# Optimization experiments

Hardware: AMD Instinct MI355X
Metric: run time of the kernel (lower is better)

The kernel has to match this reference:

```python
import jax, jax.numpy as jnp
import numpy as np

N, E, D_IN, HEADS, C = 100000, 1600000, 128, 4, 32  # C = out_channels per head


def setup_inputs() -> dict:
    key = jax.random.key(0)
    ks = jax.random.split(key, 10)
    s = 1.0 / np.sqrt(D_IN)
    return {
        "x": jax.random.normal(ks[0], (N, D_IN), jnp.float32),
        "edge_index": jax.random.randint(ks[1], (2, E), 0, N, jnp.int64),
        "Wq": jax.random.normal(ks[2], (D_IN, HEADS * C), jnp.float32) * s,
        "bq": jnp.zeros((HEADS * C,), jnp.float32),
        "Wk": jax.random.normal(ks[3], (D_IN, HEADS * C), jnp.float32) * s,
        "bk": jnp.zeros((HEADS * C,), jnp.float32),
        "Wv": jax.random.normal(ks[4], (D_IN, HEADS * C), jnp.float32) * s,
        "bv": jnp.zeros((HEADS * C,), jnp.float32),
        "Wskip": jax.random.normal(ks[5], (D_IN, HEADS * C), jnp.float32) * s,
        "bskip": jnp.zeros((HEADS * C,), jnp.float32),
    }


def reference(x, edge_index, Wq, bq, Wk, bk, Wv, bv, Wskip, bskip):
    n = x.shape[0]
    src, dst = edge_index[0], edge_index[1]  # message flows src (j) -> dst (i)
    q = (x @ Wq + bq).reshape(n, HEADS, C)
    k = (x @ Wk + bk).reshape(n, HEADS, C)
    v = (x @ Wv + bv).reshape(n, HEADS, C)

    # per-edge attention logits [E, H]
    alpha = jnp.einsum('ehc,ehc->eh', q[dst], k[src]) / jnp.sqrt(jnp.float32(C))

    # segment softmax over incoming edges of each target node
    m = jax.ops.segment_max(alpha, dst, num_segments=n)          # [N, H]
    p = jnp.exp(alpha - m[dst])                                   # [E, H]
    z = jax.ops.segment_sum(p, dst, num_segments=n)               # [N, H]
    w = p / (z[dst] + 1e-16)                                      # [E, H]

    # softmax-weighted scatter aggregation of values
    out = jax.ops.segment_sum(v[src] * w[:, :, None], dst, num_segments=n)
    out = out.reshape(n, HEADS * C)

    # root/skip connection (beta=False default: plain add)
    out = out + x @ Wskip + bskip
    return out
```

## Files before the change

### kernel.cpp

```cpp
#include <hip/hip_runtime.h>

#define DIN 128
#define NHEADS 4
#define CH 32
#define MT 128
#define CHUNK 4096
#define NPB 256
#define EPB_IT 25

#define ST_H 136

typedef _Float16 h8 __attribute__((ext_vector_type(8)));
typedef _Float16 h2 __attribute__((ext_vector_type(2)));
typedef float f4 __attribute__((ext_vector_type(4)));

__global__ __launch_bounds__(256) void prep_w(
    const float* __restrict__ Wq, const float* __restrict__ Wk,
    const float* __restrict__ Wv, const float* __restrict__ Wsk,
    _Float16* __restrict__ wt)
{
    int i = blockIdx.x * 256 + threadIdx.x;
    if (i >= 4 * 16384) return;
    int mat = i >> 14;
    int rem = i & 16383;
    int n  = rem >> 7;
    int kk = rem & 127;
    const float* W = (mat == 0) ? Wq : (mat == 1) ? Wk : (mat == 2) ? Wv : Wsk;
    wt[i] = (_Float16)W[kk * 128 + n];
}

__global__ __launch_bounds__(256) void qkvs_mat(
    const float* __restrict__ x, const _Float16* __restrict__ wt,
    const float* __restrict__ bq, const float* __restrict__ bk,
    const float* __restrict__ bv, const float* __restrict__ bsk,
    _Float16* __restrict__ qh, _Float16* __restrict__ kvh,
    _Float16* __restrict__ skiph, int N)
{
    __shared__ _Float16 Sbuf[17408];
    const int t = threadIdx.x;
    const int mat = blockIdx.x;
    const int rowBase = blockIdx.y * MT;

    for (int i = t; i < MT * 16; i += 256) {
        int r  = i >> 4;
        int c8 = i & 15;
        int gr = rowBase + r;
        _Float16 h[8];
        if (gr < N) {
            float4 f0 = reinterpret_cast<const float4*>(x)[(size_t)gr * 32 + c8 * 2];
            float4 f1 = reinterpret_cast<const float4*>(x)[(size_t)gr * 32 + c8 * 2 + 1];
            h[0] = (_Float16)f0.x; h[1] = (_Float16)f0.y;
            h[2] = (_Float16)f0.z; h[3] = (_Float16)f0.w;
            h[4] = (_Float16)f1.x; h[5] = (_Float16)f1.y;
            h[6] = (_Float16)f1.z; h[7] = (_Float16)f1.w;
        } else {
            #pragma unroll
            for (int j = 0; j < 8; ++j) h[j] = (_Float16)0.f;
        }
        *reinterpret_cast<uint4*>(&Sbuf[r * 128 + ((c8 ^ (r & 7)) << 3)]) =
            *reinterpret_cast<uint4*>(h);
    }
    __syncthreads();

    const int wid  = t >> 6;
    const int l    = t & 63;
    const int lm   = l & 15;
    const int quad = l >> 4;

    const _Float16* __restrict__ Bsrc = wt + (size_t)mat * 16384;

    f4 acc[2][8];
    #pragma unroll
    for (int ms = 0; ms < 2; ++ms)
        #pragma unroll
        for (int nt = 0; nt < 8; ++nt)
            acc[ms][nt] = (f4){0.f, 0.f, 0.f, 0.f};

    #pragma unroll
    for (int kq = 0; kq < 4; ++kq) {
        const int c8 = kq * 4 + quad;
        const int k0 = c8 << 3;
        h8 a0 = *reinterpret_cast<const h8*>(
            &Sbuf[(wid * 32 + lm) * 128 + ((c8 ^ (lm & 7)) << 3)]);
        h8 a1 = *reinterpret_cast<const h8*>(
            &Sbuf[(wid * 32 + 16 + lm) * 128 + ((c8 ^ (lm & 7)) << 3)]);
        #pragma unroll
        for (int nt = 0; nt < 8; ++nt) {
            h8 b = *reinterpret_cast<const h8*>(
                &Bsrc[(size_t)(nt * 16 + lm) * 128 + k0]);
            acc[0][nt] = __builtin_amdgcn_mfma_f32_16x16x32_f16(a0, b, acc[0][nt], 0, 0, 0);
            acc[1][nt] = __builtin_amdgcn_mfma_f32_16x16x32_f16(a1, b, acc[1][nt], 0, 0, 0);
        }
    }
    __syncthreads();

    const float* bias = (mat == 0) ? bq : (mat == 1) ? bk : (mat == 2) ? bv : bsk;

    #pragma unroll
    for (int ms = 0; ms < 2; ++ms) {
        #pragma unroll
        for (int nt = 0; nt < 8; ++nt) {
            int col = nt * 16 + lm;
            float bsv = bias[col];
            int row = wid * 32 + ms * 16 + quad * 4;
            #pragma unroll
            for (int i2 = 0; i2 < 4; ++i2)
                Sbuf[(row + i2) * ST_H + col] = (_Float16)(acc[ms][nt][i2] + bsv);
        }
    }
    __syncthreads();

    if (mat == 0 || mat == 3) {
        _Float16* __restrict__ dst = (mat == 0) ? qh : skiph;
        for (int j = t; j < 2048; j += 256) {
            int r  = j >> 4;
            int c0 = (j & 15) << 3;
            int gr = rowBase + r;
            if (gr < N)
                *reinterpret_cast<uint4*>(&dst[(size_t)gr * 128 + c0]) =
                    *reinterpret_cast<const uint4*>(&Sbuf[r * ST_H + c0]);
        }
    } else {
        const int koff = (mat == 2) ? 4 : 0;
        for (int j = t; j < 4096; j += 256) {
            int r = j >> 5;
            int g = j & 31;
            int gr = rowBase + r;
            if (gr < N)
                *reinterpret_cast<uint2*>(&kvh[(size_t)gr * 256 + g * 8 + koff]) =
                    *reinterpret_cast<const uint2*>(&Sbuf[r * ST_H + g * 4]);
        }
    }
}

__global__ __launch_bounds__(256) void bucket_hist(
    const int* __restrict__ ei, int* __restrict__ bcnt, int E, int nb)
{
    __shared__ int lds[512];
    for (int b = threadIdx.x; b < nb; b += 256) lds[b] = 0;
    __syncthreads();
    for (long long i = (long long)blockIdx.x * 256 + threadIdx.x; i < E;
         i += (long long)gridDim.x * 256)
        atomicAdd(&lds[ei[(size_t)E + i] >> 8], 1);
    __syncthreads();
    for (int b = threadIdx.x; b < nb; b += 256)
        if (lds[b]) atomicAdd(&bcnt[b], lds[b]);
}

__global__ __launch_bounds__(512) void scan_buckets(
    const int* __restrict__ bcnt, int* __restrict__ boff,
    int* __restrict__ bcur, int nb)
{
    __shared__ int ws[8];
    int t = threadIdx.x, lane = t & 63, wid = t >> 6;
    int v = (t < nb) ? bcnt[t] : 0;
    int s = v;
    #pragma unroll
    for (int off = 1; off < 64; off <<= 1) {
        int n = __shfl_up(s, off);
        if (lane >= off) s += n;
    }
    if (lane == 63) ws[wid] = s;
    __syncthreads();
    int add = 0;
    for (int w = 0; w < wid; ++w) add += ws[w];
    int excl = s - v + add;
    if (t < nb) { boff[t] = excl; bcur[t] = excl; }
    if (t == nb - 1) boff[nb] = excl + v;
}

__global__ __launch_bounds__(256) void bucket_scatter(
    const int* __restrict__ ei, int* __restrict__ bcur,
    uint2* __restrict__ pairs, int E, int nb)
{
    __shared__ int cnt[512];
    int t = threadIdx.x;
    for (int b = t; b < nb; b += 256) cnt[b] = 0;
    __syncthreads();

    long long e0 = (long long)blockIdx.x * (256 * EPB_IT);
    int ps[EPB_IT], pd[EPB_IT];
    #pragma unroll
    for (int j = 0; j < EPB_IT; ++j) {
        long long e = e0 + j * 256 + t;
        if (e < E) {
            ps[j] = ei[e];
            pd[j] = ei[(size_t)E + e];
            atomicAdd(&cnt[pd[j] >> 8], 1);
        } else pd[j] = -1;
    }
    __syncthreads();
    for (int b = t; b < nb; b += 256) {
        int c = cnt[b];
        if (c) cnt[b] = atomicAdd(&bcur[b], c);
    }
    __syncthreads();
    #pragma unroll
    for (int j = 0; j < EPB_IT; ++j) {
        if (pd[j] >= 0) {
            int pos = atomicAdd(&cnt[pd[j] >> 8], 1);
            pairs[pos] = make_uint2((unsigned)ps[j], (unsigned)pd[j]);
        }
    }
}

__global__ __launch_bounds__(256) void bucket_counts(
    const uint2* __restrict__ pairs, const int* __restrict__ boff,
    int* __restrict__ counts, int N)
{
    __shared__ int cnt[NPB];
    int b = blockIdx.x, t = threadIdx.x;
    cnt[t] = 0;
    __syncthreads();
    int s = boff[b], e = boff[b + 1];
    for (int i = s + t; i < e; i += 256)
        atomicAdd(&cnt[pairs[i].y & (NPB - 1)], 1);
    __syncthreads();
    int node = b * NPB + t;
    if (node < N) counts[node] = cnt[t];
}

__global__ __launch_bounds__(256) void chunk_sums(
    const int* __restrict__ counts, int* __restrict__ partials, int N)
{
    int b = blockIdx.x, t = threadIdx.x;
    int base = b * CHUNK + t * 16;
    int s = 0;
    #pragma unroll
    for (int j = 0; j < 16; ++j) {
        int i = base + j;
        if (i < N) s += counts[i];
    }
    #pragma unroll
    for (int off = 1; off < 64; off <<= 1) s += __shfl_xor(s, off);
    __shared__ int ws[4];
    int lane = t & 63, wid = t >> 6;
    if (lane == 0) ws[wid] = s;
    __syncthreads();
    if (t == 0) partials[b] = ws[0] + ws[1] + ws[2] + ws[3];
}

__global__ __launch_bounds__(256) void scan_chunks(
    const int* __restrict__ partials, int* __restrict__ chunkoff, int nch)
{
    __shared__ int ws[4];
    int t = threadIdx.x, lane = t & 63, wid = t >> 6;
    int v = (t < nch) ? partials[t] : 0;
    int s = v;
    #pragma unroll
    for (int off = 1; off < 64; off <<= 1) {
        int n = __shfl_up(s, off);
        if (lane >= off) s += n;
    }
    if (lane == 63) ws[wid] = s;
    __syncthreads();
    int add = 0;
    for (int w = 0; w < wid; ++w) add += ws[w];
    if (t < nch) chunkoff[t] = s - v + add;
}

__global__ __launch_bounds__(256) void scan_write(
    const int* __restrict__ counts, const int* __restrict__ chunkoff,
    int* __restrict__ rowptr, int N)
{
    int b = blockIdx.x, t = threadIdx.x;
    int base = b * CHUNK + t * 16;
    int vals[16];
    int s = 0;
    #pragma unroll
    for (int j = 0; j < 16; ++j) {
        int i = base + j;
        vals[j] = (i < N) ? counts[i] : 0;
        s += vals[j];
    }
    int lane = t & 63, wid = t >> 6;
    int incl = s;
    #pragma unroll
    for (int off = 1; off < 64; off <<= 1) {
        int n = __shfl_up(incl, off);
        if (lane >= off) incl += n;
    }
    __shared__ int ws[4];
    if (lane == 63) ws[wid] = incl;
    __syncthreads();
    int add = chunkoff[b];
    for (int w = 0; w < wid; ++w) add += ws[w];
    int run = incl - s + add;
    #pragma unroll
    for (int j = 0; j < 16; ++j) {
        int i = base + j;
        if (i < N) rowptr[i + 1] = run + vals[j];
        run += vals[j];
    }
    if (b == 0 && t == 0) rowptr[0] = 0;
}

__global__ __launch_bounds__(256) void bucket_place(
    const uint2* __restrict__ pairs, const int* __restrict__ boff,
    const int* __restrict__ rowptr, int* __restrict__ sorted, int N)
{
    __shared__ int cur[NPB];
    int b = blockIdx.x, t = threadIdx.x;
    int node = b * NPB + t;
    cur[t] = (node < N) ? rowptr[node] : 0;
    __syncthreads();
    int s = boff[b], e = boff[b + 1];
    for (int i = s + t; i < e; i += 256) {
        uint2 pr = pairs[i];
        int pos = atomicAdd(&cur[pr.y & (NPB - 1)], 1);
        sorted[pos] = (int)pr.x;
    }
}

__device__ inline float4 cvt4(unsigned lo, unsigned hi) {
    union { unsigned u[2]; _Float16 h[4]; } c;
    c.u[0] = lo; c.u[1] = hi;
    return make_float4((float)c.h[0], (float)c.h[1], (float)c.h[2], (float)c.h[3]);
}

__device__ inline h2 as_h2(unsigned u) {
    union { unsigned u; h2 h; } c;
    c.u = u;
    return c.h;
}

__global__ __launch_bounds__(256) void node_aggregate(
    const _Float16* __restrict__ q, const _Float16* __restrict__ kv,
    const _Float16* __restrict__ skiph,
    const int* __restrict__ rowptr, const int* __restrict__ srcs,
    float* __restrict__ out, int N)
{
    int gid  = blockIdx.x * 256 + threadIdx.x;
    int node = gid >> 5;
    if (node >= N) return;
    int l = gid & 31;

    uint2 qu = reinterpret_cast<const uint2*>(q + (size_t)node * 128)[l];
    h2 qa = as_h2(qu.x), qb = as_h2(qu.y);

    float4 acc = make_float4(0.f, 0.f, 0.f, 0.f);
    float z = 0.f;

    const uint4* kv4 = reinterpret_cast<const uint4*>(kv);
    const float SC = 0.17677669529663687f;
    int e0 = rowptr[node], e1 = rowptr[node + 1];
    int e = e0;

    for (; e + 8 <= e1; e += 8) {
        int s[8];
        #pragma unroll
        for (int j = 0; j < 8; ++j) s[j] = srcs[e + j];
        uint4 r[8];
        #pragma unroll
        for (int j = 0; j < 8; ++j) r[j] = kv4[(size_t)s[j] * 32 + l];

        float sv[8];
        #pragma unroll
        for (int j = 0; j < 8; ++j) {
            sv[j] = __builtin_amdgcn_fdot2(qa, as_h2(r[j].x),
                    __builtin_amdgcn_fdot2(qb, as_h2(r[j].y), 0.f, false), false);
        }
        #pragma unroll
        for (int j = 0; j < 8; ++j) sv[j] += __shfl_xor(sv[j], 1);
        #pragma unroll
        for (int j = 0; j < 8; ++j) sv[j] += __shfl_xor(sv[j], 2);
        #pragma unroll
        for (int j = 0; j < 8; ++j) sv[j] += __shfl_xor(sv[j], 4);

        #pragma unroll
        for (int j = 0; j < 8; ++j) {
            float p = __expf(sv[j] * SC);
            float4 v = cvt4(r[j].z, r[j].w);
            z += p;
            acc.x += p * v.x; acc.y += p * v.y;
            acc.z += p * v.z; acc.w += p * v.w;
        }
    }
    for (; e + 4 <= e1; e += 4) {
        int s0 = srcs[e], s1 = srcs[e + 1], s2 = srcs[e + 2], s3 = srcs[e + 3];
        uint4 r0 = kv4[(size_t)s0 * 32 + l];
        uint4 r1 = kv4[(size_t)s1 * 32 + l];
        uint4 r2 = kv4[(size_t)s2 * 32 + l];
        uint4 r3 = kv4[(size_t)s3 * 32 + l];
        float sa = __builtin_amdgcn_fdot2(qa, as_h2(r0.x),
                   __builtin_amdgcn_fdot2(qb, as_h2(r0.y), 0.f, false), false);
        float sb = __builtin_amdgcn_fdot2(qa, as_h2(r1.x),
                   __builtin_amdgcn_fdot2(qb, as_h2(r1.y), 0.f, false), false);
        float sc = __builtin_amdgcn_fdot2(qa, as_h2(r2.x),
                   __builtin_amdgcn_fdot2(qb, as_h2(r2.y), 0.f, false), false);
        float sd = __builtin_amdgcn_fdot2(qa, as_h2(r3.x),
                   __builtin_amdgcn_fdot2(qb, as_h2(r3.y), 0.f, false), false);
        sa += __shfl_xor(sa, 1); sb += __shfl_xor(sb, 1);
        sc += __shfl_xor(sc, 1); sd += __shfl_xor(sd, 1);
        sa += __shfl_xor(sa, 2); sb += __shfl_xor(sb, 2);
        sc += __shfl_xor(sc, 2); sd += __shfl_xor(sd, 2);
        sa += __shfl_xor(sa, 4); sb += __shfl_xor(sb, 4);
        sc += __shfl_xor(sc, 4); sd += __shfl_xor(sd, 4);
        float pa = __expf(sa * SC), pb = __expf(sb * SC);
        float pc = __expf(sc * SC), pdd = __expf(sd * SC);
        float4 v0 = cvt4(r0.z, r0.w);
        float4 v1 = cvt4(r1.z, r1.w);
        float4 v2 = cvt4(r2.z, r2.w);
        float4 v3 = cvt4(r3.z, r3.w);
        z += (pa + pb) + (pc + pdd);
        acc.x += pa * v0.x + pb * v1.x + pc * v2.x + pdd * v3.x;
        acc.y += pa * v0.y + pb * v1.y + pc * v2.y + pdd * v3.y;
        acc.z += pa * v0.z + pb * v1.z + pc * v2.z + pdd * v3.z;
        acc.w += pa * v0.w + pb * v1.w + pc * v2.w + pdd * v3.w;
    }
    for (; e < e1; ++e) {
        int s0 = srcs[e];
        uint4 r0 = kv4[(size_t)s0 * 32 + l];
        float sa = __builtin_amdgcn_fdot2(qa, as_h2(r0.x),
                   __builtin_amdgcn_fdot2(qb, as_h2(r0.y), 0.f, false), false);
        sa += __shfl_xor(sa, 1);
        sa += __shfl_xor(sa, 2);
        sa += __shfl_xor(sa, 4);
        float pa = __expf(sa * SC);
        float4 v0 = cvt4(r0.z, r0.w);
        z += pa;
        acc.x += pa * v0.x; acc.y += pa * v0.y;
        acc.z += pa * v0.z; acc.w += pa * v0.w;
    }

    uint2 su = reinterpret_cast<const uint2*>(skiph + (size_t)node * 128)[l];
    float4 sk = cvt4(su.x, su.y);
    float inv = 1.f / (z + 1e-16f);
    float4 o;
    o.x = sk.x + acc.x * inv; o.y = sk.y + acc.y * inv;
    o.z = sk.z + acc.z * inv; o.w = sk.w + acc.w * inv;
    reinterpret_cast<float4*>(out)[(size_t)node * 32 + l] = o;
}

extern "C" void kernel_launch(void* const* d_in, const int* in_sizes, int n_in,
                              void* d_out, int out_size, void* d_ws, size_t ws_size,
                              hipStream_t stream)
{
    const float* x   = (const float*)d_in[0];
    const int*   ei  = (const int*)d_in[1];
    const float* Wq  = (const float*)d_in[2];
    const float* bq  = (const float*)d_in[3];
    const float* Wk  = (const float*)d_in[4];
    const float* bk  = (const float*)d_in[5];
    const float* Wv  = (const float*)d_in[6];
    const float* bv  = (const float*)d_in[7];
    const float* Wsk = (const float*)d_in[8];
    const float* bsk = (const float*)d_in[9];
    float* out = (float*)d_out;

    const int N = in_sizes[0] / DIN;
    const int E = in_sizes[1] / 2;
    const int nb = (N + NPB - 1) / NPB;

    _Float16* qh    = (_Float16*)d_ws;
    _Float16* kvh   = qh + (size_t)N * DIN;
    _Float16* skiph = kvh + (size_t)N * 256;
    _Float16* wt    = skiph + (size_t)N * DIN;
    uint2* pairs  = (uint2*)(wt + 4 * 16384);
    int* sorted   = (int*)(pairs + (size_t)E);
    int* counts   = sorted + E;
    int* rowptr   = counts + N;
    int* bcnt     = rowptr + (N + 1);
    int* boff     = bcnt + 512;
    int* bcur     = boff + 513;
    int* partials = bcur + 512;
    int* chunkoff = partials + 256;

    hipMemsetAsync(bcnt, 0, 512 * sizeof(int), stream);

    prep_w<<<(4 * 16384 + 255) / 256, 256, 0, stream>>>(Wq, Wk, Wv, Wsk, wt);

    dim3 ggrid(4, (N + MT - 1) / MT);
    qkvs_mat<<<ggrid, 256, 0, stream>>>(x, wt, bq, bk, bv, bsk,
                                        qh, kvh, skiph, N);

    bucket_hist<<<256, 256, 0, stream>>>(ei, bcnt, E, nb);
    scan_buckets<<<1, 512, 0, stream>>>(bcnt, boff, bcur, nb);
    int sb = (E + 256 * EPB_IT - 1) / (256 * EPB_IT);
    bucket_scatter<<<sb, 256, 0, stream>>>(ei, bcur, pairs, E, nb);
    bucket_counts<<<nb, 256, 0, stream>>>(pairs, boff, counts, N);

    int nch = (N + CHUNK - 1) / CHUNK;
    chunk_sums<<<nch, 256, 0, stream>>>(counts, partials, N);
    scan_chunks<<<1, 256, 0, stream>>>(partials, chunkoff, nch);
    scan_write<<<nch, 256, 0, stream>>>(counts, chunkoff, rowptr, N);

    bucket_place<<<nb, 256, 0, stream>>>(pairs, boff, rowptr, sorted, N);

    int ab = (N * 32 + 255) / 256;
    node_aggregate<<<ab, 256, 0, stream>>>(qh, kvh, skiph, rowptr, sorted, out, N);
}
```

Measured before the change: 413.2 us.

## Fuse bucket count, scan and placement into one kernel; split K/V buffers

Replaces the five-kernel CSR build (bucket_counts, chunk_sums, scan_chunks, scan_write, bucket_place) with a single bucket_finalize kernel. Each bucket computes its per-node counts, scans them locally and places edges, using the bucket's global offset as the base. Edge pairs are packed into one 32-bit word (src<<8 | dst low byte), which halves scatter and read traffic but assumes src fits in 24 bits. It also splits the interleaved K/V layout into separate K and V arrays, so each edge now needs two 8-byte gathers instead of one 16-byte gather, and it drops the 4-wide tail loop in aggregation.

```diff
diff --git a/kernel.cpp b/kernel.cpp
--- a/kernel.cpp
+++ b/kernel.cpp
@@ -4,7 +4,6 @@
 #define NHEADS 4
 #define CH 32
 #define MT 128
-#define CHUNK 4096
 #define NPB 256
 #define EPB_IT 25
 
@@ -33,8 +32,8 @@
     const float* __restrict__ x, const _Float16* __restrict__ wt,
     const float* __restrict__ bq, const float* __restrict__ bk,
     const float* __restrict__ bv, const float* __restrict__ bsk,
-    _Float16* __restrict__ qh, _Float16* __restrict__ kvh,
-    _Float16* __restrict__ skiph, int N)
+    _Float16* __restrict__ qh, _Float16* __restrict__ kh,
+    _Float16* __restrict__ vh, _Float16* __restrict__ skiph, int N)
 {
     __shared__ _Float16 Sbuf[17408];
     const int t = threadIdx.x;
@@ -110,26 +109,15 @@
     }
     __syncthreads();
 
-    if (mat == 0 || mat == 3) {
-        _Float16* __restrict__ dst = (mat == 0) ? qh : skiph;
-        for (int j = t; j < 2048; j += 256) {
-            int r  = j >> 4;
-            int c0 = (j & 15) << 3;
-            int gr = rowBase + r;
-            if (gr < N)
-                *reinterpret_cast<uint4*>(&dst[(size_t)gr * 128 + c0]) =
-                    *reinterpret_cast<const uint4*>(&Sbuf[r * ST_H + c0]);
-        }
-    } else {
-        const int koff = (mat == 2) ? 4 : 0;
-        for (int j = t; j < 4096; j += 256) {
-            int r = j >> 5;
-            int g = j & 31;
-            int gr = rowBase + r;
-            if (gr < N)
-                *reinterpret_cast<uint2*>(&kvh[(size_t)gr * 256 + g * 8 + koff]) =
-                    *reinterpret_cast<const uint2*>(&Sbuf[r * ST_H + g * 4]);
-        }
+    _Float16* __restrict__ dst = (mat == 0) ? qh : (mat == 1) ? kh
+                               : (mat == 2) ? vh : skiph;
+    for (int j = t; j < 2048; j += 256) {
+        int r  = j >> 4;
+        int c0 = (j & 15) << 3;
+        int gr = rowBase + r;
+        if (gr < N)
+            *reinterpret_cast<uint4*>(&dst[(size_t)gr * 128 + c0]) =
+                *reinterpret_cast<const uint4*>(&Sbuf[r * ST_H + c0]);
     }
 }
 
@@ -171,7 +159,7 @@
 
 __global__ __launch_bounds__(256) void bucket_scatter(
     const int* __restrict__ ei, int* __restrict__ bcur,
-    uint2* __restrict__ pairs, int E, int nb)
+    unsigned* __restrict__ pairs, int E, int nb)
 {
     __shared__ int cnt[512];
     int t = threadIdx.x;
@@ -199,116 +187,50 @@
     for (int j = 0; j < EPB_IT; ++j) {
         if (pd[j] >= 0) {
             int pos = atomicAdd(&cnt[pd[j] >> 8], 1);
-            pairs[pos] = make_uint2((unsigned)ps[j], (unsigned)pd[j]);
-        }
-    }
-}
-
-__global__ __launch_bounds__(256) void bucket_counts(
-    const uint2* __restrict__ pairs, const int* __restrict__ boff,
-    int* __restrict__ counts, int N)
+            pairs[pos] = ((unsigned)ps[j] << 8) | ((unsigned)pd[j] & 255u);
+        }
+    }
+}
+
+__global__ __launch_bounds__(256) void bucket_finalize(
+    const unsigned* __restrict__ pairs, const int* __restrict__ boff,
+    int* __restrict__ rowptr, int* __restrict__ sorted, int N, int nb)
 {
     __shared__ int cnt[NPB];
+    __shared__ int cur[NPB];
+    __shared__ int ws[4];
     int b = blockIdx.x, t = threadIdx.x;
     cnt[t] = 0;
     __syncthreads();
-    int s = boff[b], e = boff[b + 1];
-    for (int i = s + t; i < e; i += 256)
-        atomicAdd(&cnt[pairs[i].y & (NPB - 1)], 1);
-    __syncthreads();
-    int node = b * NPB + t;
-    if (node < N) counts[node] = cnt[t];
-}
-
-__global__ __launch_bounds__(256) void chunk_sums(
-    const int* __restrict__ counts, int* __restrict__ partials, int N)
-{
-    int b = blockIdx.x, t = threadIdx.x;
-    int base = b * CHUNK + t * 16;
-    int s = 0;
-    #pragma unroll
-    for (int j = 0; j < 16; ++j) {
-        int i = base + j;
-        if (i < N) s += counts[i];
-    }
-    #pragma unroll
-    for (int off = 1; off < 64; off <<= 1) s += __shfl_xor(s, off);
-    __shared__ int ws[4];
+    int s0 = boff[b], e0 = boff[b + 1];
+    for (int i = s0 + t; i < e0; i += 256)
+        atomicAdd(&cnt[pairs[i] & (NPB - 1)], 1);
+    __syncthreads();
+
+    int v = cnt[t];
     int lane = t & 63, wid = t >> 6;
-    if (lane == 0) ws[wid] = s;
-    __syncthreads();
-    if (t == 0) partials[b] = ws[0] + ws[1] + ws[2] + ws[3];
-}
-
-__global__ __launch_bounds__(256) void scan_chunks(
-    const int* __restrict__ partials, int* __restrict__ chunkoff, int nch)
-{
-    __shared__ int ws[4];
-    int t = threadIdx.x, lane = t & 63, wid = t >> 6;
-    int v = (t < nch) ? partials[t] : 0;
-    int s = v;
-    #pragma unroll
-    for (int off = 1; off < 64; off <<= 1) {
-        int n = __shfl_up(s, off);
-        if (lane >= off) s += n;
-    }
-    if (lane == 63) ws[wid] = s;
-    __syncthreads();
-    int add = 0;
-    for (int w = 0; w < wid; ++w) add += ws[w];
-    if (t < nch) chunkoff[t] = s - v + add;
-}
-
-__global__ __launch_bounds__(256) void scan_write(
-    const int* __restrict__ counts, const int* __restrict__ chunkoff,
-    int* __restrict__ rowptr, int N)
-{
-    int b = blockIdx.x, t = threadIdx.x;
-    int base = b * CHUNK + t * 16;
-    int vals[16];
-    int s = 0;
-    #pragma unroll
-    for (int j = 0; j < 16; ++j) {
-        int i = base + j;
-        vals[j] = (i < N) ? counts[i] : 0;
-        s += vals[j];
-    }
-    int lane = t & 63, wid = t >> 6;
-    int incl = s;
+    int incl = v;
     #pragma unroll
     for (int off = 1; off < 64; off <<= 1) {
         int n = __shfl_up(incl, off);
         if (lane >= off) incl += n;
     }
-    __shared__ int ws[4];
     if (lane == 63) ws[wid] = incl;
     __syncthreads();
-    int add = chunkoff[b];
+    int add = 0;
     for (int w = 0; w < wid; ++w) add += ws[w];
-    int run = incl - s + add;
-    #pragma unroll
-    for (int j = 0; j < 16; ++j) {
-        int i = base + j;
-        if (i < N) rowptr[i + 1] = run + vals[j];
-        run += vals[j];
-    }
-    if (b == 0 && t == 0) rowptr[0] = 0;
-}
-
-__global__ __launch_bounds__(256) void bucket_place(
-    const uint2* __restrict__ pairs, const int* __restrict__ boff,
-    const int* __restrict__ rowptr, int* __restrict__ sorted, int N)
-{
-    __shared__ int cur[NPB];
-    int b = blockIdx.x, t = threadIdx.x;
+    int base = s0 + (incl - v) + add;
+
     int node = b * NPB + t;
-    cur[t] = (node < N) ? rowptr[node] : 0;
-    __syncthreads();
-    int s = boff[b], e = boff[b + 1];
-    for (int i = s + t; i < e; i += 256) {
-        uint2 pr = pairs[i];
-        int pos = atomicAdd(&cur[pr.y & (NPB - 1)], 1);
-        sorted[pos] = (int)pr.x;
+    if (node < N) rowptr[node] = base;
+    if (b == nb - 1 && t == 0) rowptr[N] = boff[nb];
+    cur[t] = base;
+    __syncthreads();
+
+    for (int i = s0 + t; i < e0; i += 256) {
+        unsigned pr = pairs[i];
+        int pos = atomicAdd(&cur[pr & (NPB - 1)], 1);
+        sorted[pos] = (int)(pr >> 8);
     }
 }
 
@@ -325,8 +247,8 @@
 }
 
 __global__ __launch_bounds__(256) void node_aggregate(
-    const _Float16* __restrict__ q, const _Float16* __restrict__ kv,
-    const _Float16* __restrict__ skiph,
+    const _Float16* __restrict__ q, const _Float16* __restrict__ kh,
+    const _Float16* __restrict__ vh, const _Float16* __restrict__ skiph,
     const int* __restrict__ rowptr, const int* __restrict__ srcs,
     float* __restrict__ out, int N)
 {
@@ -341,7 +263,8 @@
     float4 acc = make_float4(0.f, 0.f, 0.f, 0.f);
     float z = 0.f;
 
-    const uint4* kv4 = reinterpret_cast<const uint4*>(kv);
+    const uint2* k2 = reinterpret_cast<const uint2*>(kh);
+    const uint2* v2 = reinterpret_cast<const uint2*>(vh);
     const float SC = 0.17677669529663687f;
     int e0 = rowptr[node], e1 = rowptr[node + 1];
     int e = e0;
@@ -350,15 +273,17 @@
         int s[8];
         #pragma unroll
         for (int j = 0; j < 8; ++j) s[j] = srcs[e + j];
-        uint4 r[8];
-        #pragma unroll
-        for (int j = 0; j < 8; ++j) r[j] = kv4[(size_t)s[j] * 32 + l];
+        uint2 kr[8], vr[8];
+        #pragma unroll
+        for (int j = 0; j < 8; ++j) kr[j] = k2[(size_t)s[j] * 32 + l];
+        #pragma unroll
+        for (int j = 0; j < 8; ++j) vr[j] = v2[(size_t)s[j] * 32 + l];
 
         float sv[8];
         #pragma unroll
         for (int j = 0; j < 8; ++j) {
-            sv[j] = __builtin_amdgcn_fdot2(qa, as_h2(r[j].x),
-                    __builtin_amdgcn_fdot2(qb, as_h2(r[j].y), 0.f, false), false);
+            sv[j] = __builtin_amdgcn_fdot2(qa, as_h2(kr[j].x),
+                    __builtin_amdgcn_fdot2(qb, as_h2(kr[j].y), 0.f, false), false);
         }
         #pragma unroll
         for (int j = 0; j < 8; ++j) sv[j] += __shfl_xor(sv[j], 1);
@@ -370,54 +295,23 @@
         #pragma unroll
         for (int j = 0; j < 8; ++j) {
             float p = __expf(sv[j] * SC);
-            float4 v = cvt4(r[j].z, r[j].w);
+            float4 v = cvt4(vr[j].x, vr[j].y);
             z += p;
             acc.x += p * v.x; acc.y += p * v.y;
             acc.z += p * v.z; acc.w += p * v.w;
         }
     }
-    for (; e + 4 <= e1; e += 4) {
-        int s0 = srcs[e], s1 = srcs[e + 1], s2 = srcs[e + 2], s3 = srcs[e + 3];
-        uint4 r0 = kv4[(size_t)s0 * 32 + l];
-        uint4 r1 = kv4[(size_t)s1 * 32 + l];
-        uint4 r2 = kv4[(size_t)s2 * 32 + l];
-        uint4 r3 = kv4[(size_t)s3 * 32 + l];
-        float sa = __builtin_amdgcn_fdot2(qa, as_h2(r0.x),
-                   __builtin_amdgcn_fdot2(qb, as_h2(r0.y), 0.f, false), false);
-        float sb = __builtin_amdgcn_fdot2(qa, as_h2(r1.x),
-                   __builtin_amdgcn_fdot2(qb, as_h2(r1.y), 0.f, false), false);
-        float sc = __builtin_amdgcn_fdot2(qa, as_h2(r2.x),
-                   __builtin_amdgcn_fdot2(qb, as_h2(r2.y), 0.f, false), false);
-        float sd = __builtin_amdgcn_fdot2(qa, as_h2(r3.x),
-                   __builtin_amdgcn_fdot2(qb, as_h2(r3.y), 0.f, false), false);
-        sa += __shfl_xor(sa, 1); sb += __shfl_xor(sb, 1);
-        sc += __shfl_xor(sc, 1); sd += __shfl_xor(sd, 1);
-        sa += __shfl_xor(sa, 2); sb += __shfl_xor(sb, 2);
-        sc += __shfl_xor(sc, 2); sd += __shfl_xor(sd, 2);
-        sa += __shfl_xor(sa, 4); sb += __shfl_xor(sb, 4);
-        sc += __shfl_xor(sc, 4); sd += __shfl_xor(sd, 4);
-        float pa = __expf(sa * SC), pb = __expf(sb * SC);
-        float pc = __expf(sc * SC), pdd = __expf(sd * SC);
-        float4 v0 = cvt4(r0.z, r0.w);
-        float4 v1 = cvt4(r1.z, r1.w);
-        float4 v2 = cvt4(r2.z, r2.w);
-        float4 v3 = cvt4(r3.z, r3.w);
-        z += (pa + pb) + (pc + pdd);
-        acc.x += pa * v0.x + pb * v1.x + pc * v2.x + pdd * v3.x;
-        acc.y += pa * v0.y + pb * v1.y + pc * v2.y + pdd * v3.y;
-        acc.z += pa * v0.z + pb * v1.z + pc * v2.z + pdd * v3.z;
-        acc.w += pa * v0.w + pb * v1.w + pc * v2.w + pdd * v3.w;
-    }
     for (; e < e1; ++e) {
         int s0 = srcs[e];
-        uint4 r0 = kv4[(size_t)s0 * 32 + l];
-        float sa = __builtin_amdgcn_fdot2(qa, as_h2(r0.x),
-                   __builtin_amdgcn_fdot2(qb, as_h2(r0.y), 0.f, false), false);
+        uint2 kr = k2[(size_t)s0 * 32 + l];
+        uint2 vr = v2[(size_t)s0 * 32 + l];
+        float sa = __builtin_amdgcn_fdot2(qa, as_h2(kr.x),
+                   __builtin_amdgcn_fdot2(qb, as_h2(kr.y), 0.f, false), false);
         sa += __shfl_xor(sa, 1);
         sa += __shfl_xor(sa, 2);
         sa += __shfl_xor(sa, 4);
         float pa = __expf(sa * SC);
-        float4 v0 = cvt4(r0.z, r0.w);
+        float4 v0 = cvt4(vr.x, vr.y);
         z += pa;
         acc.x += pa * v0.x; acc.y += pa * v0.y;
         acc.z += pa * v0.z; acc.w += pa * v0.w;
@@ -453,18 +347,16 @@
     const int nb = (N + NPB - 1) / NPB;
 
     _Float16* qh    = (_Float16*)d_ws;
-    _Float16* kvh   = qh + (size_t)N * DIN;
-    _Float16* skiph = kvh + (size_t)N * 256;
+    _Float16* kh    = qh + (size_t)N * DIN;
+    _Float16* vh    = kh + (size_t)N * DIN;
+    _Float16* skiph = vh + (size_t)N * DIN;
     _Float16* wt    = skiph + (size_t)N * DIN;
-    uint2* pairs  = (uint2*)(wt + 4 * 16384);
+    unsigned* pairs = (unsigned*)(wt + 4 * 16384);
     int* sorted   = (int*)(pairs + (size_t)E);
-    int* counts   = sorted + E;
-    int* rowptr   = counts + N;
+    int* rowptr   = sorted + E;
     int* bcnt     = rowptr + (N + 1);
     int* boff     = bcnt + 512;
     int* bcur     = boff + 513;
-    int* partials = bcur + 512;
-    int* chunkoff = partials + 256;
 
     hipMemsetAsync(bcnt, 0, 512 * sizeof(int), stream);
 
@@ -472,21 +364,14 @@
 
     dim3 ggrid(4, (N + MT - 1) / MT);
     qkvs_mat<<<ggrid, 256, 0, stream>>>(x, wt, bq, bk, bv, bsk,
-                                        qh, kvh, skiph, N);
+                                        qh, kh, vh, skiph, N);
 
     bucket_hist<<<256, 256, 0, stream>>>(ei, bcnt, E, nb);
     scan_buckets<<<1, 512, 0, stream>>>(bcnt, boff, bcur, nb);
     int sb = (E + 256 * EPB_IT - 1) / (256 * EPB_IT);
     bucket_scatter<<<sb, 256, 0, stream>>>(ei, bcur, pairs, E, nb);
-    bucket_counts<<<nb, 256, 0, stream>>>(pairs, boff, counts, N);
-
-    int nch = (N + CHUNK - 1) / CHUNK;
-    chunk_sums<<<nch, 256, 0, stream>>>(counts, partials, N);
-    scan_chunks<<<1, 256, 0, stream>>>(partials, chunkoff, nch);
-    scan_write<<<nch, 256, 0, stream>>>(counts, chunkoff, rowptr, N);
-
-    bucket_place<<<nb, 256, 0, stream>>>(pairs, boff, rowptr, sorted, N);
+    bucket_finalize<<<nb, 256, 0, stream>>>(pairs, boff, rowptr, sorted, N, nb);
 
     int ab = (N * 32 + 255) / 256;
-    node_aggregate<<<ab, 256, 0, stream>>>(qh, kvh, skiph, rowptr, sorted, out, N);
-}
+    node_aggregate<<<ab, 256, 0, stream>>>(qh, kh, vh, skiph, rowptr, sorted, out, N);
+}
```

Result: faster. 401.9 us (-2.7%).
